# Performance work log

Measured on AMD Instinct MI355X. Metric: run time of the kernel, lower is better.

The kernel has to match this reference:

```python
import jax, jax.numpy as jnp
import numpy as np

N, K, M = 4096, 128, 512  # conformers, dihedrals, atoms


def setup_inputs() -> dict:
    key = jax.random.key(0)
    k1, k2 = jax.random.split(key)
    inp = jax.random.normal(k1, (N, K), dtype=jnp.float32)          # target dihedral deltas (rad)
    pos0 = jax.random.normal(k2, (N, M, 3), dtype=jnp.float32)      # initial conformer coordinates
    base = jnp.arange(K, dtype=jnp.int32)
    # chain molecule: dihedral k defined by atoms (k, k+1, k+2, k+3)
    angles = jnp.stack([base, base + 1, base + 2, base + 3], axis=1)  # (K, 4)
    # rdkit toBeMovedIdxList on a chain for bond (k+1, k+2): atoms k+3 .. M-1 move
    move_mask = jnp.arange(M)[None, :] > (base + 2)[:, None]          # (K, M) bool
    return {"input": inp, "pos0": pos0, "angles": angles, "move_mask": move_mask}


def _rot_matrix(theta, axis):
    # rdkit Transform3D::SetRotation: R = (1-cos)*aa^T + [[c,-sZ,sY],[sZ,c,-sX],[-sY,sX,c]]
    cosT = jnp.cos(theta)
    sinT = jnp.sin(theta)
    t = 1.0 - cosT
    outer = t[:, None, None] * axis[:, :, None] * axis[:, None, :]   # (N,3,3)
    X, Y, Z = axis[:, 0], axis[:, 1], axis[:, 2]
    mat1 = jnp.stack(
        [cosT, -sinT * Z, sinT * Y,
         sinT * Z, cosT, -sinT * X,
         -sinT * Y, sinT * X, cosT], axis=1
    ).reshape(-1, 3, 3)
    return outer + mat1


def _step(pos, x):
    ang, mask, theta = x                       # (4,), (M,), (N,)
    p = jnp.take(pos, ang, axis=1)             # (N,4,3) gather of i,j,k,l atoms
    rIJ = p[:, 1] - p[:, 0]
    rJK = p[:, 2] - p[:, 1]
    rKL = p[:, 3] - p[:, 2]
    nIJK = jnp.cross(rIJ, rJK)
    nJKL = jnp.cross(rJK, rKL)
    m = jnp.cross(nIJK, rJK)
    nrm = lambda v: jnp.linalg.norm(v, axis=-1)
    sin_arg = jnp.sum(m * nJKL, axis=-1) / (nrm(nJKL) * nrm(m))
    cos_arg = jnp.sum(nIJK * nJKL, axis=-1) / (nrm(nIJK) * nrm(nJKL))
    values = theta + jnp.arctan2(sin_arg, cos_arg)   # rotation angle per conformer
    begin = p[:, 1]                                   # rotation axis origin (atom j)
    d = p[:, 2] - p[:, 1]
    # torch.nn.functional.normalize with eps=1e-12
    axis = d / jnp.maximum(jnp.linalg.norm(d, axis=-1, keepdims=True), 1e-12)
    R = _rot_matrix(values, axis)                     # (N,3,3)
    rotated = jnp.einsum('nij,nmj->nmi', R, pos - begin[:, None, :]) + begin[:, None, :]
    pos = jnp.where(mask[None, :, None], rotated, pos)
    return pos, None


def reference(input, pos0, angles, move_mask):
    xs = (angles, move_mask, input.T)                 # scan over K dihedrals (sequential recurrence)
    pos, _ = jax.lax.scan(_step, pos0, xs)
    return pos
```

## Files before the change

kernel.cpp:

```cpp
#include <hip/hip_runtime.h>


#define NK 128
#define NM 512
#define NMOL 4096
#define TPB 256
#define MPB 4

struct Aff { float qw, qx, qy, qz, tx, ty, tz; };

__device__ __forceinline__ void qrot(float qw, float qx, float qy, float qz,
                                     float vx, float vy, float vz,
                                     float& ox, float& oy, float& oz) {
    const float ux = qy*vz - qz*vy + qw*vx;
    const float uy = qz*vx - qx*vz + qw*vy;
    const float uz = qx*vy - qy*vx + qw*vz;
    ox = vx + 2.f*(qy*uz - qz*uy);
    oy = vy + 2.f*(qz*ux - qx*uz);
    oz = vz + 2.f*(qx*uy - qy*ux);
}

__device__ __forceinline__ Aff aff_compose(const Aff& Q, const Aff& P) {
    Aff r;
    r.qw = Q.qw*P.qw - Q.qx*P.qx - Q.qy*P.qy - Q.qz*P.qz;
    r.qx = Q.qw*P.qx + Q.qx*P.qw + Q.qy*P.qz - Q.qz*P.qy;
    r.qy = Q.qw*P.qy - Q.qx*P.qz + Q.qy*P.qw + Q.qz*P.qx;
    r.qz = Q.qw*P.qz + Q.qx*P.qy - Q.qy*P.qx + Q.qz*P.qw;
    float rx, ry, rz;
    qrot(Q.qw, Q.qx, Q.qy, Q.qz, P.tx, P.ty, P.tz, rx, ry, rz);
    r.tx = rx + Q.tx; r.ty = ry + Q.ty; r.tz = rz + Q.tz;
    return r;
}

__device__ __forceinline__ void qnorm(Aff& a) {
    const float r = rsqrtf(a.qw*a.qw + a.qx*a.qx + a.qy*a.qy + a.qz*a.qz);
    a.qw *= r; a.qx *= r; a.qy *= r; a.qz *= r;
}

__device__ __forceinline__ Aff build_B(const float* a, float th) {
    const float ijx=a[3]-a[0], ijy=a[4]-a[1],  ijz=a[5]-a[2];
    const float jkx=a[6]-a[3], jky=a[7]-a[4],  jkz=a[8]-a[5];
    const float klx=a[9]-a[6], kly=a[10]-a[7], klz=a[11]-a[8];
    const float n1x=ijy*jkz-ijz*jky, n1y=ijz*jkx-ijx*jkz, n1z=ijx*jky-ijy*jkx;
    const float n2x=jky*klz-jkz*kly, n2y=jkz*klx-jkx*klz, n2z=jkx*kly-jky*klx;
    const float mx =n1y*jkz-n1z*jky, my =n1z*jkx-n1x*jkz, mz =n1x*jky-n1y*jkx;
    const float dmn=mx*n2x+my*n2y+mz*n2z;
    const float dnn=n1x*n2x+n1y*n2y+n1z*n2z;
    const float Lm =mx*mx+my*my+mz*mz;
    const float L1 =n1x*n1x+n1y*n1y+n1z*n1z;
    const float L2 =n2x*n2x+n2y*n2y+n2z*n2z;
    float sphi = dmn*rsqrtf(Lm*L2);
    float cphi = dnn*rsqrtf(L1*L2);
    const float rn = rsqrtf(sphi*sphi + cphi*cphi);
    sphi *= rn; cphi *= rn;
    float sth, cth; sincosf(th, &sth, &cth);
    const float c = cth*cphi - sth*sphi;
    const float s = sth*cphi + cth*sphi;
    const float Ljk = jkx*jkx + jky*jky + jkz*jkz;
    const float inva = rsqrtf(fmaxf(Ljk, 1e-24f));
    const float ax = jkx*inva, ay = jky*inva, az = jkz*inva;
    const float hc = sqrtf(fmaxf(0.f, 0.5f*(1.f + c)));
    const float hs = copysignf(sqrtf(fmaxf(0.f, 0.5f*(1.f - c))), s);
    Aff b;
    b.qw = hc; b.qx = hs*ax; b.qy = hs*ay; b.qz = hs*az;
    float rx, ry, rz;
    qrot(b.qw, b.qx, b.qy, b.qz, a[3], a[4], a[5], rx, ry, rz);
    b.tx = a[3] - rx; b.ty = a[4] - ry; b.tz = a[5] - rz;
    return b;
}

#define SHFL_AFF_UP(D, S, off)                                           \
    D.qw = __shfl_up(S.qw, off, 64); D.qx = __shfl_up(S.qx, off, 64);    \
    D.qy = __shfl_up(S.qy, off, 64); D.qz = __shfl_up(S.qz, off, 64);    \
    D.tx = __shfl_up(S.tx, off, 64); D.ty = __shfl_up(S.ty, off, 64);    \
    D.tz = __shfl_up(S.tz, off, 64);

__global__ __launch_bounds__(TPB, 4) void dihedral_quat_scan_kernel(
    const float* __restrict__ theta,
    const float* __restrict__ pos0,
    float* __restrict__ out)
{
    const int tid  = threadIdx.x;
    const int lane = tid & 63;
    const int wid  = tid >> 6;
    const int mol  = blockIdx.x * MPB + wid;
    const float4* __restrict__ pb4 = (const float4*)(pos0 + (size_t)mol * (NM*3));
    float4*       __restrict__ ob4 = (float4*)(out  + (size_t)mol * (NM*3));

    __shared__ float sA[MPB][400];
    __shared__ float sO[MPB][400];

    float4* sA4 = (float4*)sA[wid];
    for (int i = lane; i < 99; i += 64) sA4[i] = pb4[i];
    const float2 th2 = ((const float2*)(theta + (size_t)mol * NK))[lane];

    const int t0 = lane, t1 = 64 + lane;
    const bool has2 = (t1 < 95);
    float4 Ta0, Ta1, Ta2, Tb0, Tb1, Tb2;
    { const int b = 99 + 3*t0; Ta0 = pb4[b]; Ta1 = pb4[b+1]; Ta2 = pb4[b+2]; }
    if (has2) { const int b = 99 + 3*t1; Tb0 = pb4[b]; Tb1 = pb4[b+1]; Tb2 = pb4[b+2]; }

    __syncthreads();

    float A[15];
    const float* ap = &sA[wid][lane * 6];
    #pragma unroll
    for (int i = 0; i < 15; ++i) A[i] = ap[i];

    Aff Bev = build_B(&A[0], th2.x);
    Aff Bod = build_B(&A[3], th2.y);
    Aff S   = aff_compose(Bev, Bod);

    #pragma unroll
    for (int off = 1; off < 64; off <<= 1) {
        Aff Q; SHFL_AFF_UP(Q, S, off);
        if (lane >= off) S = aff_compose(Q, S);
    }
    Aff E; SHFL_AFF_UP(E, S, 1);
    if (lane == 0) { E.qw = 1.f; E.qx = E.qy = E.qz = 0.f; E.tx = E.ty = E.tz = 0.f; }
    Aff Pe = aff_compose(E, Bev);
    qnorm(Pe); qnorm(S);

    {
        float ox, oy, oz;
        float* op = &sO[wid][lane * 6 + 9];
        qrot(Pe.qw, Pe.qx, Pe.qy, Pe.qz, A[9], A[10], A[11], ox, oy, oz);
        op[0] = ox + Pe.tx; op[1] = oy + Pe.ty; op[2] = oz + Pe.tz;
        qrot(S.qw, S.qx, S.qy, S.qz, A[12], A[13], A[14], ox, oy, oz);
        op[3] = ox + S.tx;  op[4] = oy + S.ty;  op[5] = oz + S.tz;
    }
    if (lane < 9) sO[wid][lane] = sA[wid][lane];
    if (lane == 63) {
        float ox, oy, oz;
        qrot(S.qw, S.qx, S.qy, S.qz, sA[wid][393], sA[wid][394], sA[wid][395], ox, oy, oz);
        sO[wid][393] = ox + S.tx; sO[wid][394] = oy + S.ty; sO[wid][395] = oz + S.tz;
    }

    Aff F;
    F.qw = __shfl(S.qw, 63, 64); F.qx = __shfl(S.qx, 63, 64);
    F.qy = __shfl(S.qy, 63, 64); F.qz = __shfl(S.qz, 63, 64);
    F.tx = __shfl(S.tx, 63, 64); F.ty = __shfl(S.ty, 63, 64);
    F.tz = __shfl(S.tz, 63, 64);
    const float f00 = 1.f - 2.f*(F.qy*F.qy + F.qz*F.qz);
    const float f01 = 2.f*(F.qx*F.qy - F.qw*F.qz);
    const float f02 = 2.f*(F.qx*F.qz + F.qw*F.qy);
    const float f10 = 2.f*(F.qx*F.qy + F.qw*F.qz);
    const float f11 = 1.f - 2.f*(F.qx*F.qx + F.qz*F.qz);
    const float f12 = 2.f*(F.qy*F.qz - F.qw*F.qx);
    const float f20 = 2.f*(F.qx*F.qz - F.qw*F.qy);
    const float f21 = 2.f*(F.qy*F.qz + F.qw*F.qx);
    const float f22 = 1.f - 2.f*(F.qx*F.qx + F.qy*F.qy);

    __syncthreads();

    const float4* sO4 = (const float4*)sO[wid];
    for (int i = lane; i < 99; i += 64) ob4[i] = sO4[i];

    #define TAIL_EMIT(b, va, vb, vc)                                          \
    do {                                                                      \
        const float x0=va.x, y0=va.y, z0=va.z;                                \
        const float x1=va.w, y1=vb.x, z1=vb.y;                                \
        const float x2=vb.z, y2=vb.w, z2=vc.x;                                \
        const float x3=vc.y, y3=vc.z, z3=vc.w;                                \
        float4 o0, o1, o2;                                                    \
        o0.x = f00*x0+f01*y0+f02*z0+F.tx; o0.y = f10*x0+f11*y0+f12*z0+F.ty;   \
        o0.z = f20*x0+f21*y0+f22*z0+F.tz; o0.w = f00*x1+f01*y1+f02*z1+F.tx;   \
        o1.x = f10*x1+f11*y1+f12*z1+F.ty; o1.y = f20*x1+f21*y1+f22*z1+F.tz;   \
        o1.z = f00*x2+f01*y2+f02*z2+F.tx; o1.w = f10*x2+f11*y2+f12*z2+F.ty;   \
        o2.x = f20*x2+f21*y2+f22*z2+F.tz; o2.y = f00*x3+f01*y3+f02*z3+F.tx;   \
        o2.z = f10*x3+f11*y3+f12*z3+F.ty; o2.w = f20*x3+f21*y3+f22*z3+F.tz;   \
        ob4[(b)] = o0; ob4[(b)+1] = o1; ob4[(b)+2] = o2;                      \
    } while (0)

    TAIL_EMIT(99 + 3*t0, Ta0, Ta1, Ta2);
    if (has2) TAIL_EMIT(99 + 3*t1, Tb0, Tb1, Tb2);
    #undef TAIL_EMIT
}

extern "C" void kernel_launch(void* const* d_in, const int* in_sizes, int n_in,
                              void* d_out, int out_size, void* d_ws, size_t ws_size,
                              hipStream_t stream) {
    const float* theta = (const float*)d_in[0];
    const float* pos0  = (const float*)d_in[1];
    float* out = (float*)d_out;
    dihedral_quat_scan_kernel<<<NMOL / MPB, TPB, 0, stream>>>(theta, pos0, out);
}
```

Before: 19.08 us.

## Split scan head and rigid tail transform into two kernels via workspace

```diff
diff --git a/kernel.cpp b/kernel.cpp
--- a/kernel.cpp
+++ b/kernel.cpp
@@ -4,8 +4,6 @@
 #define NK 128
 #define NM 512
 #define NMOL 4096
-#define TPB 256
-#define MPB 4
 
 struct Aff { float qw, qx, qy, qz, tx, ty, tz; };
 
@@ -75,35 +73,28 @@
     D.tx = __shfl_up(S.tx, off, 64); D.ty = __shfl_up(S.ty, off, 64);    \
     D.tz = __shfl_up(S.tz, off, 64);
 
-__global__ __launch_bounds__(TPB, 4) void dihedral_quat_scan_kernel(
+__global__ __launch_bounds__(64) void dihedral_scan_head_kernel(
     const float* __restrict__ theta,
     const float* __restrict__ pos0,
-    float* __restrict__ out)
+    float* __restrict__ out,
+    float* __restrict__ ws)
 {
-    const int tid  = threadIdx.x;
-    const int lane = tid & 63;
-    const int wid  = tid >> 6;
-    const int mol  = blockIdx.x * MPB + wid;
+    const int lane = threadIdx.x;
+    const int mol  = blockIdx.x;
     const float4* __restrict__ pb4 = (const float4*)(pos0 + (size_t)mol * (NM*3));
     float4*       __restrict__ ob4 = (float4*)(out  + (size_t)mol * (NM*3));
 
-    __shared__ float sA[MPB][400];
-    __shared__ float sO[MPB][400];
+    __shared__ float sA[400];
+    __shared__ float sO[400];
 
-    float4* sA4 = (float4*)sA[wid];
-    for (int i = lane; i < 99; i += 64) sA4[i] = pb4[i];
+    float4* sA4 = (float4*)sA;
+    sA4[lane] = pb4[lane];
+    if (lane < 35) sA4[64 + lane] = pb4[64 + lane];
     const float2 th2 = ((const float2*)(theta + (size_t)mol * NK))[lane];
-
-    const int t0 = lane, t1 = 64 + lane;
-    const bool has2 = (t1 < 95);
-    float4 Ta0, Ta1, Ta2, Tb0, Tb1, Tb2;
-    { const int b = 99 + 3*t0; Ta0 = pb4[b]; Ta1 = pb4[b+1]; Ta2 = pb4[b+2]; }
-    if (has2) { const int b = 99 + 3*t1; Tb0 = pb4[b]; Tb1 = pb4[b+1]; Tb2 = pb4[b+2]; }
-
     __syncthreads();
 
     float A[15];
-    const float* ap = &sA[wid][lane * 6];
+    const float* ap = &sA[lane * 6];
     #pragma unroll
     for (int i = 0; i < 15; ++i) A[i] = ap[i];
 
@@ -123,58 +114,69 @@
 
     {
         float ox, oy, oz;
-        float* op = &sO[wid][lane * 6 + 9];
+        float* op = &sO[lane * 6 + 9];
         qrot(Pe.qw, Pe.qx, Pe.qy, Pe.qz, A[9], A[10], A[11], ox, oy, oz);
         op[0] = ox + Pe.tx; op[1] = oy + Pe.ty; op[2] = oz + Pe.tz;
         qrot(S.qw, S.qx, S.qy, S.qz, A[12], A[13], A[14], ox, oy, oz);
         op[3] = ox + S.tx;  op[4] = oy + S.ty;  op[5] = oz + S.tz;
     }
-    if (lane < 9) sO[wid][lane] = sA[wid][lane];
+    if (lane < 9) sO[lane] = sA[lane];
     if (lane == 63) {
         float ox, oy, oz;
-        qrot(S.qw, S.qx, S.qy, S.qz, sA[wid][393], sA[wid][394], sA[wid][395], ox, oy, oz);
-        sO[wid][393] = ox + S.tx; sO[wid][394] = oy + S.ty; sO[wid][395] = oz + S.tz;
+        qrot(S.qw, S.qx, S.qy, S.qz, sA[393], sA[394], sA[395], ox, oy, oz);
+        sO[393] = ox + S.tx; sO[394] = oy + S.ty; sO[395] = oz + S.tz;
+        const float qw=S.qw, qx=S.qx, qy=S.qy, qz=S.qz;
+        float4 r0, r1, r2;
+        r0.x = 1.f - 2.f*(qy*qy + qz*qz);
+        r0.y = 2.f*(qx*qy - qw*qz);
+        r0.z = 2.f*(qx*qz + qw*qy);
+        r0.w = S.tx;
+        r1.x = 2.f*(qx*qy + qw*qz);
+        r1.y = 1.f - 2.f*(qx*qx + qz*qz);
+        r1.z = 2.f*(qy*qz - qw*qx);
+        r1.w = S.ty;
+        r2.x = 2.f*(qx*qz - qw*qy);
+        r2.y = 2.f*(qy*qz + qw*qx);
+        r2.z = 1.f - 2.f*(qx*qx + qy*qy);
+        r2.w = S.tz;
+        float4* wp = (float4*)(ws + (size_t)mol * 12);
+        wp[0] = r0; wp[1] = r1; wp[2] = r2;
     }
-
-    Aff F;
-    F.qw = __shfl(S.qw, 63, 64); F.qx = __shfl(S.qx, 63, 64);
-    F.qy = __shfl(S.qy, 63, 64); F.qz = __shfl(S.qz, 63, 64);
-    F.tx = __shfl(S.tx, 63, 64); F.ty = __shfl(S.ty, 63, 64);
-    F.tz = __shfl(S.tz, 63, 64);
-    const float f00 = 1.f - 2.f*(F.qy*F.qy + F.qz*F.qz);
-    const float f01 = 2.f*(F.qx*F.qy - F.qw*F.qz);
-    const float f02 = 2.f*(F.qx*F.qz + F.qw*F.qy);
-    const float f10 = 2.f*(F.qx*F.qy + F.qw*F.qz);
-    const float f11 = 1.f - 2.f*(F.qx*F.qx + F.qz*F.qz);
-    const float f12 = 2.f*(F.qy*F.qz - F.qw*F.qx);
-    const float f20 = 2.f*(F.qx*F.qz - F.qw*F.qy);
-    const float f21 = 2.f*(F.qy*F.qz + F.qw*F.qx);
-    const float f22 = 1.f - 2.f*(F.qx*F.qx + F.qy*F.qy);
-
     __syncthreads();
 
-    const float4* sO4 = (const float4*)sO[wid];
-    for (int i = lane; i < 99; i += 64) ob4[i] = sO4[i];
+    const float4* sO4 = (const float4*)sO;
+    ob4[lane] = sO4[lane];
+    if (lane < 35) ob4[64 + lane] = sO4[64 + lane];
+}
 
-    #define TAIL_EMIT(b, va, vb, vc)                                          \
-    do {                                                                      \
-        const float x0=va.x, y0=va.y, z0=va.z;                                \
-        const float x1=va.w, y1=vb.x, z1=vb.y;                                \
-        const float x2=vb.z, y2=vb.w, z2=vc.x;                                \
-        const float x3=vc.y, y3=vc.z, z3=vc.w;                                \
-        float4 o0, o1, o2;                                                    \
-        o0.x = f00*x0+f01*y0+f02*z0+F.tx; o0.y = f10*x0+f11*y0+f12*z0+F.ty;   \
-        o0.z = f20*x0+f21*y0+f22*z0+F.tz; o0.w = f00*x1+f01*y1+f02*z1+F.tx;   \
-        o1.x = f10*x1+f11*y1+f12*z1+F.ty; o1.y = f20*x1+f21*y1+f22*z1+F.tz;   \
-        o1.z = f00*x2+f01*y2+f02*z2+F.tx; o1.w = f10*x2+f11*y2+f12*z2+F.ty;   \
-        o2.x = f20*x2+f21*y2+f22*z2+F.tz; o2.y = f00*x3+f01*y3+f02*z3+F.tx;   \
-        o2.z = f10*x3+f11*y3+f12*z3+F.ty; o2.w = f20*x3+f21*y3+f22*z3+F.tz;   \
-        ob4[(b)] = o0; ob4[(b)+1] = o1; ob4[(b)+2] = o2;                      \
-    } while (0)
+#define K2_TPB 384
+__global__ __launch_bounds__(K2_TPB) void dihedral_tail_kernel(
+    const float* __restrict__ pos0,
+    const float* __restrict__ ws,
+    float* __restrict__ out)
+{
+    const int t   = threadIdx.x;
+    const int mol = blockIdx.x;
+    const float4* __restrict__ wp = (const float4*)(ws + (size_t)mol * 12);
+    const float4 r0 = wp[0], r1 = wp[1], r2 = wp[2];
 
-    TAIL_EMIT(99 + 3*t0, Ta0, Ta1, Ta2);
-    if (has2) TAIL_EMIT(99 + 3*t1, Tb0, Tb1, Tb2);
-    #undef TAIL_EMIT
+    if (t < NM - (NK + 3) - 1) {
+        const int m = (NK + 4) + t;
+        const float* p = pos0 + (size_t)mol * (NM*3) + (size_t)m * 3;
+        float*       o = out  + (size_t)mol * (NM*3) + (size_t)m * 3;
+        const float x = p[0], y = p[1], z = p[2];
+        o[0] = r0.x*x + r0.y*y + r0.z*z + r0.w;
+        o[1] = r1.x*x + r1.y*y + r1.z*z + r1.w;
+        o[2] = r2.x*x + r2.y*y + r2.z*z + r2.w;
+    } else if (t == NM - (NK + 3) - 1) {
+        const int m = NK + 4 - 1;
+        const float* p = pos0 + (size_t)mol * (NM*3) + (size_t)m * 3;
+        float*       o = out  + (size_t)mol * (NM*3) + (size_t)m * 3;
+        const float x = p[0], y = p[1], z = p[2];
+        o[0] = r0.x*x + r0.y*y + r0.z*z + r0.w;
+        o[1] = r1.x*x + r1.y*y + r1.z*z + r1.w;
+        o[2] = r2.x*x + r2.y*y + r2.z*z + r2.w;
+    }
 }
 
 extern "C" void kernel_launch(void* const* d_in, const int* in_sizes, int n_in,
@@ -183,5 +185,7 @@
     const float* theta = (const float*)d_in[0];
     const float* pos0  = (const float*)d_in[1];
     float* out = (float*)d_out;
-    dihedral_quat_scan_kernel<<<NMOL / MPB, TPB, 0, stream>>>(theta, pos0, out);
+    float* ws  = (float*)d_ws;
+    dihedral_scan_head_kernel<<<NMOL, 64, 0, stream>>>(theta, pos0, out, ws);
+    dihedral_tail_kernel<<<NMOL, K2_TPB, 0, stream>>>(pos0, ws, out);
 }
```

After: 23.00 us. 1.21x slower.

## Process two molecules per wave with prefetch and drop block barriers

Applied to the files above, without the earlier changes.

```diff
diff --git a/kernel.cpp b/kernel.cpp
--- a/kernel.cpp
+++ b/kernel.cpp
@@ -5,7 +5,8 @@
 #define NM 512
 #define NMOL 4096
 #define TPB 256
-#define MPB 4
+#define WPB 4
+#define MPWAVE 2
 
 struct Aff { float qw, qx, qy, qz, tx, ty, tz; };
 
@@ -37,35 +38,33 @@
     a.qw *= r; a.qx *= r; a.qy *= r; a.qz *= r;
 }
 
-__device__ __forceinline__ Aff build_B(const float* a, float th) {
+__device__ __forceinline__ Aff build_step(const float* a, float th) {
     const float ijx=a[3]-a[0], ijy=a[4]-a[1],  ijz=a[5]-a[2];
     const float jkx=a[6]-a[3], jky=a[7]-a[4],  jkz=a[8]-a[5];
     const float klx=a[9]-a[6], kly=a[10]-a[7], klz=a[11]-a[8];
     const float n1x=ijy*jkz-ijz*jky, n1y=ijz*jkx-ijx*jkz, n1z=ijx*jky-ijy*jkx;
     const float n2x=jky*klz-jkz*kly, n2y=jkz*klx-jkx*klz, n2z=jkx*kly-jky*klx;
-    const float mx =n1y*jkz-n1z*jky, my =n1z*jkx-n1x*jkz, mz =n1x*jky-n1y*jkx;
-    const float dmn=mx*n2x+my*n2y+mz*n2z;
+    const float L1=n1x*n1x+n1y*n1y+n1z*n1z;
+    const float L2=n2x*n2x+n2y*n2y+n2z*n2z;
     const float dnn=n1x*n2x+n1y*n2y+n1z*n2z;
-    const float Lm =mx*mx+my*my+mz*mz;
-    const float L1 =n1x*n1x+n1y*n1y+n1z*n1z;
-    const float L2 =n2x*n2x+n2y*n2y+n2z*n2z;
-    float sphi = dmn*rsqrtf(Lm*L2);
-    float cphi = dnn*rsqrtf(L1*L2);
-    const float rn = rsqrtf(sphi*sphi + cphi*cphi);
-    sphi *= rn; cphi *= rn;
-    float sth, cth; sincosf(th, &sth, &cth);
+    const float cxx=n2y*n1z-n2z*n1y, cxy=n2z*n1x-n2x*n1z, cxz=n2x*n1y-n2y*n1x;
+    const float g  = cxx*jkx + cxy*jky + cxz*jkz;
+    const float Ljk = jkx*jkx+jky*jky+jkz*jkz;
+    const float ira = rsqrtf(fmaxf(Ljk, 1e-24f));
+    const float r12 = rsqrtf(fmaxf(L1*L2, 1e-30f));
+    const float cphi = dnn*r12;
+    const float sphi = g*r12*ira;
+    const float sth = __sinf(th), cth = __cosf(th);
     const float c = cth*cphi - sth*sphi;
     const float s = sth*cphi + cth*sphi;
-    const float Ljk = jkx*jkx + jky*jky + jkz*jkz;
-    const float inva = rsqrtf(fmaxf(Ljk, 1e-24f));
-    const float ax = jkx*inva, ay = jky*inva, az = jkz*inva;
     const float hc = sqrtf(fmaxf(0.f, 0.5f*(1.f + c)));
     const float hs = copysignf(sqrtf(fmaxf(0.f, 0.5f*(1.f - c))), s);
+    const float hsa = hs*ira;
     Aff b;
-    b.qw = hc; b.qx = hs*ax; b.qy = hs*ay; b.qz = hs*az;
+    b.qw = hc; b.qx = jkx*hsa; b.qy = jky*hsa; b.qz = jkz*hsa;
     float rx, ry, rz;
     qrot(b.qw, b.qx, b.qy, b.qz, a[3], a[4], a[5], rx, ry, rz);
-    b.tx = a[3] - rx; b.ty = a[4] - ry; b.tz = a[5] - rz;
+    b.tx = a[3]-rx; b.ty = a[4]-ry; b.tz = a[5]-rz;
     return b;
 }
 
@@ -75,40 +74,20 @@
     D.tx = __shfl_up(S.tx, off, 64); D.ty = __shfl_up(S.ty, off, 64);    \
     D.tz = __shfl_up(S.tz, off, 64);
 
-__global__ __launch_bounds__(TPB, 4) void dihedral_quat_scan_kernel(
-    const float* __restrict__ theta,
-    const float* __restrict__ pos0,
-    float* __restrict__ out)
+__device__ __forceinline__ void do_molecule(
+    const int lane, float* __restrict__ sA, float* __restrict__ sO,
+    float4* __restrict__ ob4, const float2 th2,
+    const float4 Ta0, const float4 Ta1, const float4 Ta2,
+    const float4 Tb0, const float4 Tb1, const float4 Tb2, const bool hasB)
 {
-    const int tid  = threadIdx.x;
-    const int lane = tid & 63;
-    const int wid  = tid >> 6;
-    const int mol  = blockIdx.x * MPB + wid;
-    const float4* __restrict__ pb4 = (const float4*)(pos0 + (size_t)mol * (NM*3));
-    float4*       __restrict__ ob4 = (float4*)(out  + (size_t)mol * (NM*3));
-
-    __shared__ float sA[MPB][400];
-    __shared__ float sO[MPB][400];
-
-    float4* sA4 = (float4*)sA[wid];
-    for (int i = lane; i < 99; i += 64) sA4[i] = pb4[i];
-    const float2 th2 = ((const float2*)(theta + (size_t)mol * NK))[lane];
-
-    const int t0 = lane, t1 = 64 + lane;
-    const bool has2 = (t1 < 95);
-    float4 Ta0, Ta1, Ta2, Tb0, Tb1, Tb2;
-    { const int b = 99 + 3*t0; Ta0 = pb4[b]; Ta1 = pb4[b+1]; Ta2 = pb4[b+2]; }
-    if (has2) { const int b = 99 + 3*t1; Tb0 = pb4[b]; Tb1 = pb4[b+1]; Tb2 = pb4[b+2]; }
-
-    __syncthreads();
-
-    float A[15];
-    const float* ap = &sA[wid][lane * 6];
+    float A[16];
+    const float2* ap2 = (const float2*)&sA[lane * 6];
     #pragma unroll
-    for (int i = 0; i < 15; ++i) A[i] = ap[i];
-
-    Aff Bev = build_B(&A[0], th2.x);
-    Aff Bod = build_B(&A[3], th2.y);
+    for (int i = 0; i < 7; ++i) { const float2 v = ap2[i]; A[2*i] = v.x; A[2*i+1] = v.y; }
+    A[14] = sA[lane * 6 + 14];
+
+    Aff Bev = build_step(&A[0], th2.x);
+    Aff Bod = build_step(&A[3], th2.y);
     Aff S   = aff_compose(Bev, Bod);
 
     #pragma unroll
@@ -123,17 +102,17 @@
 
     {
         float ox, oy, oz;
-        float* op = &sO[wid][lane * 6 + 9];
+        float* op = &sO[lane * 6 + 9];
         qrot(Pe.qw, Pe.qx, Pe.qy, Pe.qz, A[9], A[10], A[11], ox, oy, oz);
         op[0] = ox + Pe.tx; op[1] = oy + Pe.ty; op[2] = oz + Pe.tz;
         qrot(S.qw, S.qx, S.qy, S.qz, A[12], A[13], A[14], ox, oy, oz);
         op[3] = ox + S.tx;  op[4] = oy + S.ty;  op[5] = oz + S.tz;
     }
-    if (lane < 9) sO[wid][lane] = sA[wid][lane];
+    if (lane < 9) sO[lane] = sA[lane];
     if (lane == 63) {
         float ox, oy, oz;
-        qrot(S.qw, S.qx, S.qy, S.qz, sA[wid][393], sA[wid][394], sA[wid][395], ox, oy, oz);
-        sO[wid][393] = ox + S.tx; sO[wid][394] = oy + S.ty; sO[wid][395] = oz + S.tz;
+        qrot(S.qw, S.qx, S.qy, S.qz, sA[393], sA[394], sA[395], ox, oy, oz);
+        sO[393] = ox + S.tx; sO[394] = oy + S.ty; sO[395] = oz + S.tz;
     }
 
     Aff F;
@@ -151,10 +130,9 @@
     const float f21 = 2.f*(F.qy*F.qz + F.qw*F.qx);
     const float f22 = 1.f - 2.f*(F.qx*F.qx + F.qy*F.qy);
 
-    __syncthreads();
-
-    const float4* sO4 = (const float4*)sO[wid];
-    for (int i = lane; i < 99; i += 64) ob4[i] = sO4[i];
+    const float4* sO4 = (const float4*)sO;
+    ob4[lane] = sO4[lane];
+    if (lane < 35) ob4[64 + lane] = sO4[64 + lane];
 
     #define TAIL_EMIT(b, va, vb, vc)                                          \
     do {                                                                      \
@@ -172,9 +150,54 @@
         ob4[(b)] = o0; ob4[(b)+1] = o1; ob4[(b)+2] = o2;                      \
     } while (0)
 
-    TAIL_EMIT(99 + 3*t0, Ta0, Ta1, Ta2);
-    if (has2) TAIL_EMIT(99 + 3*t1, Tb0, Tb1, Tb2);
+    TAIL_EMIT(99 + 3*lane, Ta0, Ta1, Ta2);
+    if (hasB) TAIL_EMIT(99 + 3*(64 + lane), Tb0, Tb1, Tb2);
     #undef TAIL_EMIT
+}
+
+__global__ __launch_bounds__(TPB, 2) void dihedral_pipe2_kernel(
+    const float* __restrict__ theta,
+    const float* __restrict__ pos0,
+    float* __restrict__ out)
+{
+    const int tid  = threadIdx.x;
+    const int lane = tid & 63;
+    const int wid  = tid >> 6;
+    const int molA = blockIdx.x * (WPB * MPWAVE) + wid;
+    const int molB = molA + WPB;
+
+    const float4* __restrict__ pbA = (const float4*)(pos0 + (size_t)molA * (NM*3));
+    float4*       __restrict__ obA = (float4*)(out  + (size_t)molA * (NM*3));
+    const float4* __restrict__ pbB = (const float4*)(pos0 + (size_t)molB * (NM*3));
+    float4*       __restrict__ obB = (float4*)(out  + (size_t)molB * (NM*3));
+
+    __shared__ float sA[WPB][400];
+    __shared__ float sO[WPB][400];
+
+    const bool hasB2 = (lane < 31);
+
+    float4 hA0 = pbA[lane];
+    float4 hA1; if (lane < 35) hA1 = pbA[64 + lane];
+    const float2 thA = ((const float2*)(theta + (size_t)molA * NK))[lane];
+    float4 hB0 = pbB[lane];
+    float4 hB1; if (lane < 35) hB1 = pbB[64 + lane];
+    const float2 thB = ((const float2*)(theta + (size_t)molB * NK))[lane];
+    float4 TaA0, TaA1, TaA2, TbA0, TbA1, TbA2;
+    { const int b = 99 + 3*lane; TaA0 = pbA[b]; TaA1 = pbA[b+1]; TaA2 = pbA[b+2]; }
+    if (hasB2) { const int b = 99 + 3*(64 + lane); TbA0 = pbA[b]; TbA1 = pbA[b+1]; TbA2 = pbA[b+2]; }
+
+    float4* sA4 = (float4*)sA[wid];
+    sA4[lane] = hA0;
+    if (lane < 35) sA4[64 + lane] = hA1;
+    do_molecule(lane, sA[wid], sO[wid], obA, thA, TaA0, TaA1, TaA2, TbA0, TbA1, TbA2, hasB2);
+
+    float4 TaB0, TaB1, TaB2, TbB0, TbB1, TbB2;
+    { const int b = 99 + 3*lane; TaB0 = pbB[b]; TaB1 = pbB[b+1]; TaB2 = pbB[b+2]; }
+    if (hasB2) { const int b = 99 + 3*(64 + lane); TbB0 = pbB[b]; TbB1 = pbB[b+1]; TbB2 = pbB[b+2]; }
+
+    sA4[lane] = hB0;
+    if (lane < 35) sA4[64 + lane] = hB1;
+    do_molecule(lane, sA[wid], sO[wid], obB, thB, TaB0, TaB1, TaB2, TbB0, TbB1, TbB2, hasB2);
 }
 
 extern "C" void kernel_launch(void* const* d_in, const int* in_sizes, int n_in,
@@ -183,5 +206,5 @@
     const float* theta = (const float*)d_in[0];
     const float* pos0  = (const float*)d_in[1];
     float* out = (float*)d_out;
-    dihedral_quat_scan_kernel<<<NMOL / MPB, TPB, 0, stream>>>(theta, pos0, out);
-}
+    dihedral_pipe2_kernel<<<NMOL / (WPB * MPWAVE), TPB, 0, stream>>>(theta, pos0, out);
+}
```

After: 18.96 us. About the same (-0.6%).

## Split wavefront into two 32-lane segments, four dihedrals per lane

Applied to the files above, without the earlier changes.

```diff
diff --git a/kernel.cpp b/kernel.cpp
--- a/kernel.cpp
+++ b/kernel.cpp
@@ -5,7 +5,8 @@
 #define NM 512
 #define NMOL 4096
 #define TPB 256
-#define MPB 4
+#define WPB 4
+#define MPW 2
 
 struct Aff { float qw, qx, qy, qz, tx, ty, tz; };
 
@@ -32,50 +33,33 @@
     return r;
 }
 
-__device__ __forceinline__ void qnorm(Aff& a) {
-    const float r = rsqrtf(a.qw*a.qw + a.qx*a.qx + a.qy*a.qy + a.qz*a.qz);
-    a.qw *= r; a.qx *= r; a.qy *= r; a.qz *= r;
-}
-
-__device__ __forceinline__ Aff build_B(const float* a, float th) {
-    const float ijx=a[3]-a[0], ijy=a[4]-a[1],  ijz=a[5]-a[2];
-    const float jkx=a[6]-a[3], jky=a[7]-a[4],  jkz=a[8]-a[5];
-    const float klx=a[9]-a[6], kly=a[10]-a[7], klz=a[11]-a[8];
-    const float n1x=ijy*jkz-ijz*jky, n1y=ijz*jkx-ijx*jkz, n1z=ijx*jky-ijy*jkx;
-    const float n2x=jky*klz-jkz*kly, n2y=jkz*klx-jkx*klz, n2z=jkx*kly-jky*klx;
-    const float mx =n1y*jkz-n1z*jky, my =n1z*jkx-n1x*jkz, mz =n1x*jky-n1y*jkx;
-    const float dmn=mx*n2x+my*n2y+mz*n2z;
-    const float dnn=n1x*n2x+n1y*n2y+n1z*n2z;
-    const float Lm =mx*mx+my*my+mz*mz;
-    const float L1 =n1x*n1x+n1y*n1y+n1z*n1z;
-    const float L2 =n2x*n2x+n2y*n2y+n2z*n2z;
-    float sphi = dmn*rsqrtf(Lm*L2);
-    float cphi = dnn*rsqrtf(L1*L2);
-    const float rn = rsqrtf(sphi*sphi + cphi*cphi);
-    sphi *= rn; cphi *= rn;
-    float sth, cth; sincosf(th, &sth, &cth);
-    const float c = cth*cphi - sth*sphi;
-    const float s = sth*cphi + cth*sphi;
-    const float Ljk = jkx*jkx + jky*jky + jkz*jkz;
-    const float inva = rsqrtf(fmaxf(Ljk, 1e-24f));
-    const float ax = jkx*inva, ay = jky*inva, az = jkz*inva;
-    const float hc = sqrtf(fmaxf(0.f, 0.5f*(1.f + c)));
-    const float hs = copysignf(sqrtf(fmaxf(0.f, 0.5f*(1.f - c))), s);
-    Aff b;
-    b.qw = hc; b.qx = hs*ax; b.qy = hs*ay; b.qz = hs*az;
-    float rx, ry, rz;
-    qrot(b.qw, b.qx, b.qy, b.qz, a[3], a[4], a[5], rx, ry, rz);
-    b.tx = a[3] - rx; b.ty = a[4] - ry; b.tz = a[5] - rz;
-    return b;
-}
-
-#define SHFL_AFF_UP(D, S, off)                                           \
-    D.qw = __shfl_up(S.qw, off, 64); D.qx = __shfl_up(S.qx, off, 64);    \
-    D.qy = __shfl_up(S.qy, off, 64); D.qz = __shfl_up(S.qz, off, 64);    \
-    D.tx = __shfl_up(S.tx, off, 64); D.ty = __shfl_up(S.ty, off, 64);    \
-    D.tz = __shfl_up(S.tz, off, 64);
-
-__global__ __launch_bounds__(TPB, 4) void dihedral_quat_scan_kernel(
+#define SHFL_AFF_UP32(D, S, off)                                         \
+    D.qw = __shfl_up(S.qw, off, 32); D.qx = __shfl_up(S.qx, off, 32);    \
+    D.qy = __shfl_up(S.qy, off, 32); D.qz = __shfl_up(S.qz, off, 32);    \
+    D.tx = __shfl_up(S.tx, off, 32); D.ty = __shfl_up(S.ty, off, 32);    \
+    D.tz = __shfl_up(S.tz, off, 32);
+
+#define BUILD_STEP(j, OUT) do {                                               \
+    const float cxx = ny[(j)+1]*nz[(j)] - nz[(j)+1]*ny[(j)];                  \
+    const float cxy = nz[(j)+1]*nx[(j)] - nx[(j)+1]*nz[(j)];                  \
+    const float cxz = nx[(j)+1]*ny[(j)] - ny[(j)+1]*nx[(j)];                  \
+    const float g   = cxx*vx[(j)+1] + cxy*vy[(j)+1] + cxz*vz[(j)+1];          \
+    const float dnn = nx[(j)]*nx[(j)+1] + ny[(j)]*ny[(j)+1] + nz[(j)]*nz[(j)+1]; \
+    const float r12 = rsqrtf(fmaxf(Ln[(j)]*Ln[(j)+1], 1e-30f));               \
+    const float ira = rsqrtf(fmaxf(Lv[(j)+1], 1e-24f));                       \
+    const float cphi = dnn*r12, sphi = g*r12*ira;                             \
+    const float sth = __sinf(th[(j)]), cth = __cosf(th[(j)]);                 \
+    const float c = cth*cphi - sth*sphi, s = sth*cphi + cth*sphi;             \
+    const float hc = sqrtf(fmaxf(0.f, 0.5f*(1.f + c)));                       \
+    const float hs = copysignf(sqrtf(fmaxf(0.f, 0.5f*(1.f - c))), s);         \
+    const float hsa = hs*ira;                                                 \
+    OUT.qw = hc; OUT.qx = vx[(j)+1]*hsa; OUT.qy = vy[(j)+1]*hsa; OUT.qz = vz[(j)+1]*hsa; \
+    float rx, ry, rz;                                                         \
+    qrot(OUT.qw, OUT.qx, OUT.qy, OUT.qz, A[3*(j)+3], A[3*(j)+4], A[3*(j)+5], rx, ry, rz); \
+    OUT.tx = A[3*(j)+3]-rx; OUT.ty = A[3*(j)+4]-ry; OUT.tz = A[3*(j)+5]-rz;   \
+} while (0)
+
+__global__ __launch_bounds__(TPB, 2) void dihedral_seg2_kernel(
     const float* __restrict__ theta,
     const float* __restrict__ pos0,
     float* __restrict__ out)
@@ -83,64 +67,101 @@
     const int tid  = threadIdx.x;
     const int lane = tid & 63;
     const int wid  = tid >> 6;
-    const int mol  = blockIdx.x * MPB + wid;
+    const int seg  = lane >> 5;
+    const int sl   = lane & 31;
+    const int mol  = blockIdx.x * (WPB * MPW) + wid * MPW + seg;
+
     const float4* __restrict__ pb4 = (const float4*)(pos0 + (size_t)mol * (NM*3));
     float4*       __restrict__ ob4 = (float4*)(out  + (size_t)mol * (NM*3));
 
-    __shared__ float sA[MPB][400];
-    __shared__ float sO[MPB][400];
-
-    float4* sA4 = (float4*)sA[wid];
-    for (int i = lane; i < 99; i += 64) sA4[i] = pb4[i];
-    const float2 th2 = ((const float2*)(theta + (size_t)mol * NK))[lane];
-
-    const int t0 = lane, t1 = 64 + lane;
-    const bool has2 = (t1 < 95);
-    float4 Ta0, Ta1, Ta2, Tb0, Tb1, Tb2;
-    { const int b = 99 + 3*t0; Ta0 = pb4[b]; Ta1 = pb4[b+1]; Ta2 = pb4[b+2]; }
-    if (has2) { const int b = 99 + 3*t1; Tb0 = pb4[b]; Tb1 = pb4[b+1]; Tb2 = pb4[b+2]; }
-
-    __syncthreads();
-
-    float A[15];
-    const float* ap = &sA[wid][lane * 6];
-    #pragma unroll
-    for (int i = 0; i < 15; ++i) A[i] = ap[i];
-
-    Aff Bev = build_B(&A[0], th2.x);
-    Aff Bod = build_B(&A[3], th2.y);
-    Aff S   = aff_compose(Bev, Bod);
-
-    #pragma unroll
-    for (int off = 1; off < 64; off <<= 1) {
-        Aff Q; SHFL_AFF_UP(Q, S, off);
-        if (lane >= off) S = aff_compose(Q, S);
-    }
-    Aff E; SHFL_AFF_UP(E, S, 1);
-    if (lane == 0) { E.qw = 1.f; E.qx = E.qy = E.qz = 0.f; E.tx = E.ty = E.tz = 0.f; }
-    Aff Pe = aff_compose(E, Bev);
-    qnorm(Pe); qnorm(S);
+    __shared__ float sA[WPB][MPW][400];
+    __shared__ float sO[WPB][MPW][400];
+
+    const bool ex = (sl < 3);
+    float4 h0 = pb4[sl], h1 = pb4[sl + 32], h2 = pb4[sl + 64];
+    float4 h3; if (ex) h3 = pb4[96 + sl];
+    const float4 th4 = ((const float4*)(theta + (size_t)mol * NK))[sl];
+    float4 T0a, T0b, T0c, T1a, T1b, T1c, T2a, T2b, T2c;
+    { const int b = 99 + 3*sl;        T0a = pb4[b]; T0b = pb4[b+1]; T0c = pb4[b+2]; }
+    { const int b = 99 + 3*(sl + 32); T1a = pb4[b]; T1b = pb4[b+1]; T1c = pb4[b+2]; }
+    const bool has3 = (sl < 31);
+    if (has3) { const int b = 99 + 3*(sl + 64); T2a = pb4[b]; T2b = pb4[b+1]; T2c = pb4[b+2]; }
+
+    float4* sA4 = (float4*)sA[wid][seg];
+    sA4[sl] = h0; sA4[sl + 32] = h1; sA4[sl + 64] = h2;
+    if (ex) sA4[96 + sl] = h3;
+
+    float A[21];
+    {
+        const float2* ap2 = (const float2*)&sA[wid][seg][sl * 12];
+        #pragma unroll
+        for (int i = 0; i < 10; ++i) { const float2 v = ap2[i]; A[2*i] = v.x; A[2*i+1] = v.y; }
+        A[20] = sA[wid][seg][sl * 12 + 20];
+    }
+
+    float vx[6], vy[6], vz[6];
+    #pragma unroll
+    for (int i = 0; i < 6; ++i) {
+        vx[i] = A[3*i+3] - A[3*i];
+        vy[i] = A[3*i+4] - A[3*i+1];
+        vz[i] = A[3*i+5] - A[3*i+2];
+    }
+    float nx[5], ny[5], nz[5], Ln[5];
+    #pragma unroll
+    for (int i = 0; i < 5; ++i) {
+        nx[i] = vy[i]*vz[i+1] - vz[i]*vy[i+1];
+        ny[i] = vz[i]*vx[i+1] - vx[i]*vz[i+1];
+        nz[i] = vx[i]*vy[i+1] - vy[i]*vx[i+1];
+        Ln[i] = nx[i]*nx[i] + ny[i]*ny[i] + nz[i]*nz[i];
+    }
+    float Lv[5];
+    #pragma unroll
+    for (int i = 1; i < 5; ++i) Lv[i] = vx[i]*vx[i] + vy[i]*vy[i] + vz[i]*vz[i];
+    const float th[4] = {th4.x, th4.y, th4.z, th4.w};
+
+    Aff B0;   BUILD_STEP(0, B0);
+    Aff Bt;   BUILD_STEP(1, Bt);
+    Aff C01  = aff_compose(B0, Bt);
+    BUILD_STEP(2, Bt);
+    Aff C012 = aff_compose(C01, Bt);
+    BUILD_STEP(3, Bt);
+    Aff S    = aff_compose(C012, Bt);
+
+    #pragma unroll
+    for (int off = 1; off < 32; off <<= 1) {
+        Aff Q; SHFL_AFF_UP32(Q, S, off);
+        if (sl >= off) S = aff_compose(Q, S);
+    }
+    Aff E; SHFL_AFF_UP32(E, S, 1);
+    if (sl == 0) { E.qw = 1.f; E.qx = E.qy = E.qz = 0.f; E.tx = E.ty = E.tz = 0.f; }
+    const Aff P0 = aff_compose(E, B0);
+    const Aff P1 = aff_compose(E, C01);
+    const Aff P2 = aff_compose(E, C012);
 
     {
         float ox, oy, oz;
-        float* op = &sO[wid][lane * 6 + 9];
-        qrot(Pe.qw, Pe.qx, Pe.qy, Pe.qz, A[9], A[10], A[11], ox, oy, oz);
-        op[0] = ox + Pe.tx; op[1] = oy + Pe.ty; op[2] = oz + Pe.tz;
-        qrot(S.qw, S.qx, S.qy, S.qz, A[12], A[13], A[14], ox, oy, oz);
-        op[3] = ox + S.tx;  op[4] = oy + S.ty;  op[5] = oz + S.tz;
-    }
-    if (lane < 9) sO[wid][lane] = sA[wid][lane];
-    if (lane == 63) {
+        float* op = &sO[wid][seg][12*sl + 9];
+        qrot(P0.qw, P0.qx, P0.qy, P0.qz, A[9],  A[10], A[11], ox, oy, oz);
+        op[0] = ox + P0.tx; op[1] = oy + P0.ty; op[2] = oz + P0.tz;
+        qrot(P1.qw, P1.qx, P1.qy, P1.qz, A[12], A[13], A[14], ox, oy, oz);
+        op[3] = ox + P1.tx; op[4] = oy + P1.ty; op[5] = oz + P1.tz;
+        qrot(P2.qw, P2.qx, P2.qy, P2.qz, A[15], A[16], A[17], ox, oy, oz);
+        op[6] = ox + P2.tx; op[7] = oy + P2.ty; op[8] = oz + P2.tz;
+        qrot(S.qw, S.qx, S.qy, S.qz, A[18], A[19], A[20], ox, oy, oz);
+        op[9] = ox + S.tx;  op[10] = oy + S.ty; op[11] = oz + S.tz;
+    }
+    if (sl < 9) sO[wid][seg][sl] = sA[wid][seg][sl];
+    if (sl == 31) {
         float ox, oy, oz;
-        qrot(S.qw, S.qx, S.qy, S.qz, sA[wid][393], sA[wid][394], sA[wid][395], ox, oy, oz);
-        sO[wid][393] = ox + S.tx; sO[wid][394] = oy + S.ty; sO[wid][395] = oz + S.tz;
+        qrot(S.qw, S.qx, S.qy, S.qz, sA[wid][seg][393], sA[wid][seg][394], sA[wid][seg][395], ox, oy, oz);
+        sO[wid][seg][393] = ox + S.tx; sO[wid][seg][394] = oy + S.ty; sO[wid][seg][395] = oz + S.tz;
     }
 
     Aff F;
-    F.qw = __shfl(S.qw, 63, 64); F.qx = __shfl(S.qx, 63, 64);
-    F.qy = __shfl(S.qy, 63, 64); F.qz = __shfl(S.qz, 63, 64);
-    F.tx = __shfl(S.tx, 63, 64); F.ty = __shfl(S.ty, 63, 64);
-    F.tz = __shfl(S.tz, 63, 64);
+    F.qw = __shfl(S.qw, 31, 32); F.qx = __shfl(S.qx, 31, 32);
+    F.qy = __shfl(S.qy, 31, 32); F.qz = __shfl(S.qz, 31, 32);
+    F.tx = __shfl(S.tx, 31, 32); F.ty = __shfl(S.ty, 31, 32);
+    F.tz = __shfl(S.tz, 31, 32);
     const float f00 = 1.f - 2.f*(F.qy*F.qy + F.qz*F.qz);
     const float f01 = 2.f*(F.qx*F.qy - F.qw*F.qz);
     const float f02 = 2.f*(F.qx*F.qz + F.qw*F.qy);
@@ -151,10 +172,9 @@
     const float f21 = 2.f*(F.qy*F.qz + F.qw*F.qx);
     const float f22 = 1.f - 2.f*(F.qx*F.qx + F.qy*F.qy);
 
-    __syncthreads();
-
-    const float4* sO4 = (const float4*)sO[wid];
-    for (int i = lane; i < 99; i += 64) ob4[i] = sO4[i];
+    const float4* sO4 = (const float4*)sO[wid][seg];
+    ob4[sl] = sO4[sl]; ob4[sl + 32] = sO4[sl + 32]; ob4[sl + 64] = sO4[sl + 64];
+    if (ex) ob4[96 + sl] = sO4[96 + sl];
 
     #define TAIL_EMIT(b, va, vb, vc)                                          \
     do {                                                                      \
@@ -172,8 +192,9 @@
         ob4[(b)] = o0; ob4[(b)+1] = o1; ob4[(b)+2] = o2;                      \
     } while (0)
 
-    TAIL_EMIT(99 + 3*t0, Ta0, Ta1, Ta2);
-    if (has2) TAIL_EMIT(99 + 3*t1, Tb0, Tb1, Tb2);
+    TAIL_EMIT(99 + 3*sl,        T0a, T0b, T0c);
+    TAIL_EMIT(99 + 3*(sl + 32), T1a, T1b, T1c);
+    if (has3) TAIL_EMIT(99 + 3*(sl + 64), T2a, T2b, T2c);
     #undef TAIL_EMIT
 }
 
@@ -183,5 +204,5 @@
     const float* theta = (const float*)d_in[0];
     const float* pos0  = (const float*)d_in[1];
     float* out = (float*)d_out;
-    dihedral_quat_scan_kernel<<<NMOL / MPB, TPB, 0, stream>>>(theta, pos0, out);
-}
+    dihedral_seg2_kernel<<<NMOL / (WPB * MPW), TPB, 0, stream>>>(theta, pos0, out);
+}
```

Measured after the change: 17.67 us. -7.4%, faster.
